# Kernel tuning notes

Measured on AMD Instinct MI355X. Metric: run time of the kernel, lower is better.

The kernel has to match this reference:

```python
import jax, jax.numpy as jnp
import numpy as np

B, CI, HW, K, C, NH, L = 512, 3, 28, 28 // 28 and 0 or 7, 1024, 16, 12
K = 7


def setup_inputs() -> dict:
    key = jax.random.key(0)
    ks = jax.random.split(key, 8)
    s = 0.02
    return {
        "x": jax.random.normal(ks[0], (B, CI, HW, HW), jnp.float32),
        "conv_w": jax.random.normal(ks[1], (C, CI, K, K), jnp.float32) * s,  # Conv2d weight [Co,Ci,k,k], shared with deconv
        "ln1_w": jnp.ones((L, C), jnp.float32),
        "ln1_b": jnp.zeros((L, C), jnp.float32),
        "wq": jax.random.normal(ks[2], (L, C, C), jnp.float32) * s,
        "wk": jax.random.normal(ks[3], (L, C, C), jnp.float32) * s,
        "wv": jax.random.normal(ks[4], (L, C, C), jnp.float32) * s,
        "ln2_w": jnp.ones((L, C), jnp.float32),
        "ln2_b": jnp.zeros((L, C), jnp.float32),
        "mlp_w": jax.random.normal(ks[5], (L, C, C), jnp.float32) * s,
        "mlp_b": jnp.zeros((L, C), jnp.float32),
        "out_w": jax.random.normal(ks[6], (C, C), jnp.float32) * s,
        "out_b": jnp.zeros((C,), jnp.float32),
        "head_num": NH,
    }


def _layernorm(x, w, b, eps=1e-5):
    m = jnp.mean(x, axis=-1, keepdims=True)
    v = jnp.var(x, axis=-1, keepdims=True)  # biased var, matches torch LayerNorm
    return (x - m) * jax.lax.rsqrt(v + eps) * w + b


def _attn(h, wq, wk, wv, nh):
    b, t, c = h.shape
    hd = c // nh
    q = (h @ wq.T).reshape(b, t, nh, hd).transpose(0, 2, 1, 3)  # [B,H,T,hd]
    k = (h @ wk.T).reshape(b, t, nh, hd).transpose(0, 2, 1, 3)
    v = (h @ wv.T).reshape(b, t, nh, hd).transpose(0, 2, 1, 3)
    scores = jnp.einsum("bhqd,bhkd->bhqk", q, k) / jnp.sqrt(jnp.float32(hd))
    mask = jnp.tril(jnp.ones((t, t), bool))
    scores = jnp.where(mask, scores, -jnp.inf)
    a = jax.nn.softmax(scores, axis=-1)
    o = jnp.einsum("bhqk,bhkd->bhqd", a, v)
    return o.transpose(0, 2, 1, 3).reshape(b, t, c)


def _forward(x, conv_w, ln1_w, ln1_b, wq, wk, wv, ln2_w, ln2_b, mlp_w, mlp_b, out_w, out_b, head_num):
    b, ci, hh, ww = x.shape
    co, _, k, _ = conv_w.shape
    # thumbnail: bilinear downsample to (k,k) (align_corners=False == half-pixel), then k-strided conv -> [B,Co]
    thumb = jax.image.resize(x, (b, ci, k, k), method="bilinear", antialias=False)
    thumb_tok = jnp.einsum("bcpq,dcpq->bd", thumb, conv_w)
    # kernel==stride conv == patchify + matmul
    hp, wp = hh // k, ww // k
    xp = x.reshape(b, ci, hp, k, wp, k)
    patches = jnp.einsum("bcipjq,dcpq->bdij", xp, conv_w).reshape(b, co, hp * wp)
    h = jnp.concatenate([thumb_tok[:, :, None], patches], axis=-1).transpose(0, 2, 1)  # [B,T=1+hp*wp,C]
    nlayers = ln1_w.shape[0]
    for l in range(nlayers):
        a = _attn(_layernorm(h, ln1_w[l], ln1_b[l]), wq[l], wk[l], wv[l], head_num)
        h = h + a
        m = _layernorm(h, ln2_w[l], ln2_b[l]) @ mlp_w[l].T + mlp_b[l]
        h = h + m
    logits = h @ out_w.T + out_b  # [B,T,C]
    # decode: ConvTranspose2d(kernel=stride=k) with shared weight; input [B,Co,1,T] -> [B,Ci,k,T*k]
    z = logits.transpose(0, 2, 1)  # [B,Co,T]
    t = z.shape[-1]
    out = jnp.einsum("bcs,cdhw->bdhsw", z, conv_w).reshape(b, ci, k, t * k)
    return out


def reference(x, conv_w, ln1_w, ln1_b, wq, wk, wv, ln2_w, ln2_b, mlp_w, mlp_b, out_w, out_b, head_num):
    return _forward(x, conv_w, ln1_w, ln1_b, wq, wk, wv, ln2_w, ln2_b, mlp_w, mlp_b, out_w, out_b, head_num)
```

## Files before the change

### kernel.cpp

```cpp
#include <hip/hip_runtime.h>


typedef unsigned short u16;
typedef short bfrag8 __attribute__((ext_vector_type(8)));
typedef float facc4 __attribute__((ext_vector_type(4)));

__device__ __forceinline__ u16 f2bf(float f) {
  union { float f; unsigned u; } x; x.f = f;
  unsigned r = x.u + 0x7fffu + ((x.u >> 16) & 1u);
  return (u16)(r >> 16);
}
__device__ __forceinline__ float bf2f(u16 h) {
  union { unsigned u; float f; } x; x.u = ((unsigned)h) << 16;
  return x.f;
}

template <int MODE>
__global__ __launch_bounds__(256) void gemm_bt(
    const u16* __restrict__ A, int lda,
    const u16* __restrict__ B0, const u16* __restrict__ B1, const u16* __restrict__ B2,
    int ldb, int K,
    void* __restrict__ outp, long long zstride, int ldo,
    const float* __restrict__ bias)
{
  __shared__ __align__(16) u16 smem[8192];
  u16* const As = smem;
  u16* const Bs = smem + 4096;

  const int m0 = blockIdx.x * 128;
  const int n0 = blockIdx.y * 128;
  const int z  = blockIdx.z;
  const u16* __restrict__ B = (z == 0) ? B0 : ((z == 1) ? B1 : B2);

  const int tid  = threadIdx.x;
  const int wave = tid >> 6;
  const int lane = tid & 63;
  const int wm   = (wave >> 1) * 64;
  const int wn   = (wave & 1) * 64;
  const int lrow = lane & 15;
  const int lquad = lane >> 4;

  facc4 acc[4][4] = {};

  int rA0, g0; { const int rp = tid >> 3, q = tid & 7, qp = q ^ (rp & 3);
                 rA0 = rp * 2 + (qp >> 2); g0 = qp & 3; }
  int rA1, g1; { const int s1 = tid + 256, rp = s1 >> 3, q = s1 & 7, qp = q ^ (rp & 3);
                 rA1 = rp * 2 + (qp >> 2); g1 = qp & 3; }
  const u16* ga0 = A + (long long)(m0 + rA0) * lda + g0 * 8;
  const u16* ga1 = A + (long long)(m0 + rA1) * lda + g1 * 8;
  const u16* gb0 = B + (long long)(n0 + rA0) * ldb + g0 * 8;
  const u16* gb1 = B + (long long)(n0 + rA1) * ldb + g1 * 8;

  const int ra = wm + lrow;
  const int pa = (((ra & 1) << 2) | lquad) ^ ((ra >> 1) & 3);
  const u16* const abase = As + (((ra >> 1) * 8 + pa) << 3);
  const int rb = wn + lrow;
  const int pb = (((rb & 1) << 2) | lquad) ^ ((rb >> 1) & 3);
  const u16* const bbase = Bs + (((rb >> 1) * 8 + pb) << 3);

  for (int k0 = 0; k0 < K; k0 += 32) {
    __builtin_amdgcn_global_load_lds((const __attribute__((address_space(1))) void*)ga0,
                                     (__attribute__((address_space(3))) void*)(As + tid * 8), 16, 0, 0);
    __builtin_amdgcn_global_load_lds((const __attribute__((address_space(1))) void*)ga1,
                                     (__attribute__((address_space(3))) void*)(As + (tid + 256) * 8), 16, 0, 0);
    __builtin_amdgcn_global_load_lds((const __attribute__((address_space(1))) void*)gb0,
                                     (__attribute__((address_space(3))) void*)(Bs + tid * 8), 16, 0, 0);
    __builtin_amdgcn_global_load_lds((const __attribute__((address_space(1))) void*)gb1,
                                     (__attribute__((address_space(3))) void*)(Bs + (tid + 256) * 8), 16, 0, 0);
    ga0 += 32; ga1 += 32; gb0 += 32; gb1 += 32;
    __syncthreads();

    bfrag8 af[4], bfr[4];
#pragma unroll
    for (int im = 0; im < 4; ++im) af[im] = *(const bfrag8*)(abase + 512 * im);
#pragma unroll
    for (int in = 0; in < 4; ++in) bfr[in] = *(const bfrag8*)(bbase + 512 * in);
#pragma unroll
    for (int im = 0; im < 4; ++im)
#pragma unroll
      for (int in = 0; in < 4; ++in)
        acc[im][in] = __builtin_amdgcn_mfma_f32_16x16x32_bf16(af[im], bfr[in], acc[im][in], 0, 0, 0);
    __syncthreads();
  }

  if (MODE == 1) {
    u16* const outb = ((u16*)outp) + zstride * z;
    u16* const Ts = smem;
#pragma unroll
    for (int half = 0; half < 2; ++half) {
      if ((wave >> 1) == half) {
#pragma unroll
        for (int in = 0; in < 4; ++in) {
          const int col = wn + in * 16 + lrow;
          const float bb = bias ? bias[n0 + col] : 0.0f;
#pragma unroll
          for (int im = 0; im < 4; ++im)
#pragma unroll
            for (int r = 0; r < 4; ++r)
              Ts[(im * 16 + lquad * 4 + r) * 128 + col] = f2bf(acc[im][in][r] + bb);
        }
      }
      __syncthreads();
#pragma unroll
      for (int it = 0; it < 4; ++it) {
        const int g = it * 256 + tid;
        const int row = g >> 4, colg = g & 15;
        *(uint4*)(outb + (long long)(m0 + half * 64 + row) * ldo + n0 + colg * 8) =
            *(const uint4*)(Ts + row * 128 + colg * 8);
      }
      __syncthreads();
    }
    return;
  }

#pragma unroll
  for (int in = 0; in < 4; ++in) {
    const int col = n0 + wn + in * 16 + lrow;
    const float bb = (MODE != 3 && bias) ? bias[col] : 0.0f;
#pragma unroll
    for (int im = 0; im < 4; ++im) {
#pragma unroll
      for (int r = 0; r < 4; ++r) {
        const int row = m0 + wm + im * 16 + lquad * 4 + r;
        const float v = acc[im][in][r] + bb;
        if (MODE == 0) {
          ((float*)outp)[(long long)row * ldo + col] = v;
        } else if (MODE == 2) {
          ((float*)outp)[(long long)row * ldo + col] += v;
        } else {
          if (col < 147) {
            const int b = row / 17, s = row - b * 17;
            const int d = col / 49, rem = col - d * 49;
            const int hk = rem / 7, wk = rem - hk * 7;
            ((float*)outp)[(long long)((b * 3 + d) * 7 + hk) * 119 + s * 7 + wk] = v;
          }
        }
      }
    }
  }
}

__global__ __launch_bounds__(256) void ln_kernel(
    const float* __restrict__ h, const float* __restrict__ w,
    const float* __restrict__ b, u16* __restrict__ out)
{
  const long long row = blockIdx.x;
  const float* __restrict__ x = h + row * 1024;
  const int t = threadIdx.x;
  float v0 = x[t], v1 = x[t + 256], v2 = x[t + 512], v3 = x[t + 768];
  float s = v0 + v1 + v2 + v3;
  float q = v0 * v0 + v1 * v1 + v2 * v2 + v3 * v3;
  for (int o = 32; o > 0; o >>= 1) { s += __shfl_down(s, o); q += __shfl_down(q, o); }
  __shared__ float ss[4], sq[4];
  const int wave = t >> 6, lane = t & 63;
  if (lane == 0) { ss[wave] = s; sq[wave] = q; }
  __syncthreads();
  const float st = ss[0] + ss[1] + ss[2] + ss[3];
  const float qt = sq[0] + sq[1] + sq[2] + sq[3];
  const float mean = st * (1.0f / 1024.0f);
  const float var = qt * (1.0f / 1024.0f) - mean * mean;
  const float inv = rsqrtf(var + 1e-5f);
  u16* o2 = out + row * 1024;
  o2[t]       = f2bf((v0 - mean) * inv * w[t]       + b[t]);
  o2[t + 256] = f2bf((v1 - mean) * inv * w[t + 256] + b[t + 256]);
  o2[t + 512] = f2bf((v2 - mean) * inv * w[t + 512] + b[t + 512]);
  o2[t + 768] = f2bf((v3 - mean) * inv * w[t + 768] + b[t + 768]);
}

__global__ __launch_bounds__(256) void attn_kernel(const u16* __restrict__ QKV,
                                                   float* __restrict__ h)
{
  const int blk = blockIdx.x;
  const int b = blk >> 4, head = blk & 15;
  __shared__ float qs[17][64], ks[17][64], vs[17][64];
  __shared__ float sc[17][20];
  const long long base = (long long)b * 17 * 1024 + head * 64;
  const u16* Q  = QKV;
  const u16* Kp = QKV + 8912896LL;
  const u16* V  = QKV + 17825792LL;

  for (int i = threadIdx.x; i < 17 * 64; i += 256) {
    const int t = i >> 6, d = i & 63;
    const long long off = base + (long long)t * 1024 + d;
    qs[t][d] = bf2f(Q[off]); ks[t][d] = bf2f(Kp[off]); vs[t][d] = bf2f(V[off]);
  }
  __syncthreads();

  for (int i = threadIdx.x; i < 289; i += 256) {
    const int tq = i / 17, tk = i % 17;
    float a = 0.0f;
    if (tk <= tq) {
#pragma unroll
      for (int d = 0; d < 64; ++d) a += qs[tq][d] * ks[tk][d];
      a *= 0.125f;
    }
    sc[tq][tk] = a;
  }
  __syncthreads();

  if (threadIdx.x < 17) {
    const int tq = threadIdx.x;
    float m = -1e30f;
    for (int tk = 0; tk <= tq; ++tk) m = fmaxf(m, sc[tq][tk]);
    float s = 0.0f;
    for (int tk = 0; tk <= tq; ++tk) { const float e = __expf(sc[tq][tk] - m); sc[tq][tk] = e; s += e; }
    const float inv = 1.0f / s;
    for (int tk = 0; tk <= tq; ++tk) sc[tq][tk] *= inv;
  }
  __syncthreads();

  for (int i = threadIdx.x; i < 17 * 64; i += 256) {
    const int tq = i >> 6, d = i & 63;
    float a = 0.0f;
    for (int tk = 0; tk <= tq; ++tk) a += sc[tq][tk] * vs[tk][d];
    h[base + (long long)tq * 1024 + d] += a;
  }
}

__global__ void build_p(const float* __restrict__ x, u16* __restrict__ P)
{
  const int n = blockIdx.x;
  const int j = threadIdx.x;
  if (j >= 160) return;
  const int b = n / 17, t = n % 17;
  float val = 0.0f;
  if (j < 147) {
    const int c = j / 49, rem = j % 49, p = rem / 7, q = rem % 7;
    const float* xb = x + (long long)(b * 3 + c) * 784;
    if (t == 0) {
      const int r = 4 * p + 1, cc = 4 * q + 1;
      val = 0.25f * (xb[r * 28 + cc] + xb[r * 28 + cc + 1] +
                     xb[(r + 1) * 28 + cc] + xb[(r + 1) * 28 + cc + 1]);
    } else {
      const int s = t - 1, ii = s >> 2, jj = s & 3;
      val = xb[(7 * ii + p) * 28 + 7 * jj + q];
    }
  }
  P[(long long)n * 160 + j] = f2bf(val);
}

__global__ __launch_bounds__(256) void cvt_conv(const float* __restrict__ cw,
                                                u16* __restrict__ Wc, u16* __restrict__ cw2)
{
  const int i = blockIdx.x * 256 + threadIdx.x;
  if (i < 163840) {
    const int d = i / 160, j = i % 160;
    Wc[i] = (j < 147) ? f2bf(cw[d * 147 + j]) : (u16)0;
  } else {
    const int i2 = i - 163840;
    if (i2 < 262144) {
      const int j = i2 / 1024, c = i2 % 1024;
      cw2[i2] = (j < 147) ? f2bf(cw[c * 147 + j]) : (u16)0;
    }
  }
}

__global__ __launch_bounds__(256) void cvt_all(
    const float* __restrict__ wq, const float* __restrict__ wk,
    const float* __restrict__ wv, const float* __restrict__ mlpw,
    const float* __restrict__ outw, u16* __restrict__ wAll)
{
  const int i = blockIdx.x * 256 + threadIdx.x;
  const int which = i >> 18;
  const int off = i & 262143;
  const float4* src;
  if (which < 48) {
    const int layer = which >> 2, sub = which & 3;
    const float* base = (sub == 0) ? wq : (sub == 1) ? wk : (sub == 2) ? wv : mlpw;
    src = (const float4*)(base + (size_t)layer * 1048576) + off;
  } else {
    src = (const float4*)outw + off;
  }
  const float4 v = *src;
  ushort4 o; o.x = f2bf(v.x); o.y = f2bf(v.y); o.z = f2bf(v.z); o.w = f2bf(v.w);
  *(ushort4*)(wAll + (size_t)which * 1048576 + (size_t)off * 4) = o;
}

__global__ __launch_bounds__(256) void cvt4(const float* __restrict__ a0, const float* __restrict__ a1,
                                            const float* __restrict__ a2, const float* __restrict__ a3,
                                            u16* __restrict__ o3, u16* __restrict__ om)
{
  const int i = blockIdx.x * 256 + threadIdx.x;
  const int which = i >> 20, off = i & 1048575;
  const float* src = (which == 0) ? a0 : (which == 1) ? a1 : (which == 2) ? a2 : a3;
  const float v = src[off];
  if (which < 3) o3[which * 1048576 + off] = f2bf(v);
  else           om[off] = f2bf(v);
}

__global__ __launch_bounds__(256) void cvtN(const float* __restrict__ in, u16* __restrict__ out, int n)
{
  const int i = blockIdx.x * 256 + threadIdx.x;
  if (i < n) out[i] = f2bf(in[i]);
}

extern "C" void kernel_launch(void* const* d_in, const int* in_sizes, int n_in,
                              void* d_out, int out_size, void* d_ws, size_t ws_size,
                              hipStream_t stream)
{
  const float* x     = (const float*)d_in[0];
  const float* convw = (const float*)d_in[1];
  const float* ln1w  = (const float*)d_in[2];
  const float* ln1b  = (const float*)d_in[3];
  const float* wq    = (const float*)d_in[4];
  const float* wk    = (const float*)d_in[5];
  const float* wv    = (const float*)d_in[6];
  const float* ln2w  = (const float*)d_in[7];
  const float* ln2b  = (const float*)d_in[8];
  const float* mlpw  = (const float*)d_in[9];
  const float* mlpb  = (const float*)d_in[10];
  const float* outw  = (const float*)d_in[11];
  const float* outb  = (const float*)d_in[12];

  char* w = (char*)d_ws;
  const bool big = (ws_size >= 213352448ULL);

  if (big) {
    float* h   = (float*)(w);
    u16* Abuf  = (u16*)(w + 35651584);
    u16* QKV   = (u16*)(w + 53477376);
    u16* wAll  = (u16*)(w + 106954752);
    u16* Wc    = (u16*)(w + 209715200);
    u16* cw2   = (u16*)(w + 210042880);
    u16* P     = (u16*)(w + 210567168);

    cvt_all<<<50176, 256, 0, stream>>>(wq, wk, wv, mlpw, outw, wAll);
    cvt_conv<<<1664, 256, 0, stream>>>(convw, Wc, cw2);
    build_p<<<8704, 192, 0, stream>>>(x, P);
    gemm_bt<0><<<dim3(68, 8, 1), 256, 0, stream>>>(P, 160, Wc, Wc, Wc, 160, 160,
                                                   (void*)h, 0LL, 1024, nullptr);
    for (int l = 0; l < 12; ++l) {
      u16* wl = wAll + (size_t)l * 4194304;
      ln_kernel<<<8704, 256, 0, stream>>>(h, ln1w + l * 1024, ln1b + l * 1024, Abuf);
      gemm_bt<1><<<dim3(68, 8, 3), 256, 0, stream>>>(Abuf, 1024, wl, wl + 1048576, wl + 2097152,
                                                     1024, 1024, (void*)QKV, 8912896LL, 1024, nullptr);
      attn_kernel<<<8192, 256, 0, stream>>>(QKV, h);
      ln_kernel<<<8704, 256, 0, stream>>>(h, ln2w + l * 1024, ln2b + l * 1024, Abuf);
      gemm_bt<2><<<dim3(68, 8, 1), 256, 0, stream>>>(Abuf, 1024, wl + 3145728, wl, wl,
                                                     1024, 1024, (void*)h, 0LL, 1024, mlpb + l * 1024);
    }
    u16* wout = wAll + (size_t)48 * 1048576;
    cvtN<<<34816, 256, 0, stream>>>(h, Abuf, 8912896);
    gemm_bt<1><<<dim3(68, 8, 1), 256, 0, stream>>>(Abuf, 1024, wout, wout, wout,
                                                   1024, 1024, (void*)QKV, 0LL, 1024, outb);
    gemm_bt<3><<<dim3(68, 2, 1), 256, 0, stream>>>(QKV, 1024, cw2, cw2, cw2,
                                                   1024, 1024, d_out, 0LL, 0, nullptr);
  } else {
    if (ws_size < 118980608ULL) return;
    float* h   = (float*)(w);
    u16* Abuf  = (u16*)(w + 35651584);
    u16* QKV   = (u16*)(w + 53477376);
    u16* wb3   = (u16*)(w + 106954752);
    u16* wmb   = (u16*)(w + 113246208);
    u16* Wc    = (u16*)(w + 115343360);
    u16* cw2   = (u16*)(w + 115671040);
    u16* P     = (u16*)(w + 116195328);

    cvt_conv<<<1664, 256, 0, stream>>>(convw, Wc, cw2);
    build_p<<<8704, 192, 0, stream>>>(x, P);
    gemm_bt<0><<<dim3(68, 8, 1), 256, 0, stream>>>(P, 160, Wc, Wc, Wc, 160, 160,
                                                   (void*)h, 0LL, 1024, nullptr);
    for (int l = 0; l < 12; ++l) {
      const size_t wo = (size_t)l * 1048576;
      cvt4<<<16384, 256, 0, stream>>>(wq + wo, wk + wo, wv + wo, mlpw + wo, wb3, wmb);
      ln_kernel<<<8704, 256, 0, stream>>>(h, ln1w + l * 1024, ln1b + l * 1024, Abuf);
      gemm_bt<1><<<dim3(68, 8, 3), 256, 0, stream>>>(Abuf, 1024, wb3, wb3 + 1048576, wb3 + 2097152,
                                                     1024, 1024, (void*)QKV, 8912896LL, 1024, nullptr);
      attn_kernel<<<8192, 256, 0, stream>>>(QKV, h);
      ln_kernel<<<8704, 256, 0, stream>>>(h, ln2w + l * 1024, ln2b + l * 1024, Abuf);
      gemm_bt<2><<<dim3(68, 8, 1), 256, 0, stream>>>(Abuf, 1024, wmb, wmb, wmb,
                                                     1024, 1024, (void*)h, 0LL, 1024, mlpb + l * 1024);
    }
    cvtN<<<34816, 256, 0, stream>>>(h, Abuf, 8912896);
    cvtN<<<4096, 256, 0, stream>>>(outw, wmb, 1048576);
    gemm_bt<1><<<dim3(68, 8, 1), 256, 0, stream>>>(Abuf, 1024, wmb, wmb, wmb,
                                                   1024, 1024, (void*)QKV, 0LL, 1024, outb);
    gemm_bt<3><<<dim3(68, 2, 1), 256, 0, stream>>>(QKV, 1024, cw2, cw2, cw2,
                                                   1024, 1024, d_out, 0LL, 0, nullptr);
  }
}
```

Before: 3.052 ms.

## Use K=64 GEMM tiles, swap grid order, drop LDS swizzle and staged bf16 store

The bf16 GEMM now loads a 64-wide K slice per iteration into separate A/B shared buffers, which halves the number of barrier pairs per tile. The grid is reordered so blockIdx.x walks N, letting consecutive blocks share the same A rows. The XOR-swizzled LDS layout is replaced with a plain row layout, and the LDS-staged coalesced bf16 epilogue for MODE 1 is replaced with direct scalar stores. The patch-embedding K is padded to 192 to fit the new tile depth. The plain layout risks LDS bank conflicts, and the scalar bf16 stores are uncoalesced.

```diff
diff --git a/kernel.cpp b/kernel.cpp
--- a/kernel.cpp
+++ b/kernel.cpp
@@ -23,12 +23,11 @@
     void* __restrict__ outp, long long zstride, int ldo,
     const float* __restrict__ bias)
 {
-  __shared__ __align__(16) u16 smem[8192];
-  u16* const As = smem;
-  u16* const Bs = smem + 4096;
-
-  const int m0 = blockIdx.x * 128;
-  const int n0 = blockIdx.y * 128;
+  __shared__ __align__(16) u16 As[8192];
+  __shared__ __align__(16) u16 Bs[8192];
+
+  const int n0 = blockIdx.x * 128;
+  const int m0 = blockIdx.y * 128;
   const int z  = blockIdx.z;
   const u16* __restrict__ B = (z == 0) ? B0 : ((z == 1) ? B1 : B2);
 
@@ -42,75 +41,44 @@
 
   facc4 acc[4][4] = {};
 
-  int rA0, g0; { const int rp = tid >> 3, q = tid & 7, qp = q ^ (rp & 3);
-                 rA0 = rp * 2 + (qp >> 2); g0 = qp & 3; }
-  int rA1, g1; { const int s1 = tid + 256, rp = s1 >> 3, q = s1 & 7, qp = q ^ (rp & 3);
-                 rA1 = rp * 2 + (qp >> 2); g1 = qp & 3; }
-  const u16* ga0 = A + (long long)(m0 + rA0) * lda + g0 * 8;
-  const u16* ga1 = A + (long long)(m0 + rA1) * lda + g1 * 8;
-  const u16* gb0 = B + (long long)(n0 + rA0) * ldb + g0 * 8;
-  const u16* gb1 = B + (long long)(n0 + rA1) * ldb + g1 * 8;
-
-  const int ra = wm + lrow;
-  const int pa = (((ra & 1) << 2) | lquad) ^ ((ra >> 1) & 3);
-  const u16* const abase = As + (((ra >> 1) * 8 + pa) << 3);
-  const int rb = wn + lrow;
-  const int pb = (((rb & 1) << 2) | lquad) ^ ((rb >> 1) & 3);
-  const u16* const bbase = Bs + (((rb >> 1) * 8 + pb) << 3);
-
-  for (int k0 = 0; k0 < K; k0 += 32) {
-    __builtin_amdgcn_global_load_lds((const __attribute__((address_space(1))) void*)ga0,
-                                     (__attribute__((address_space(3))) void*)(As + tid * 8), 16, 0, 0);
-    __builtin_amdgcn_global_load_lds((const __attribute__((address_space(1))) void*)ga1,
-                                     (__attribute__((address_space(3))) void*)(As + (tid + 256) * 8), 16, 0, 0);
-    __builtin_amdgcn_global_load_lds((const __attribute__((address_space(1))) void*)gb0,
-                                     (__attribute__((address_space(3))) void*)(Bs + tid * 8), 16, 0, 0);
-    __builtin_amdgcn_global_load_lds((const __attribute__((address_space(1))) void*)gb1,
-                                     (__attribute__((address_space(3))) void*)(Bs + (tid + 256) * 8), 16, 0, 0);
-    ga0 += 32; ga1 += 32; gb0 += 32; gb1 += 32;
+  const u16* ga[4]; const u16* gb[4];
+#pragma unroll
+  for (int j = 0; j < 4; ++j) {
+    const int s = tid + 256 * j;
+    const int t = s >> 9, s2 = s & 511;
+    const int r = s2 >> 2, c = (s2 & 3) + 4 * t;
+    ga[j] = A + (long long)(m0 + r) * lda + c * 8;
+    gb[j] = B + (long long)(n0 + r) * ldb + c * 8;
+  }
+
+  const int aoff = (wm + lrow) * 32 + lquad * 8;
+  const int boff = (wn + lrow) * 32 + lquad * 8;
+
+  for (int k0 = 0; k0 < K; k0 += 64) {
+#pragma unroll
+    for (int j = 0; j < 4; ++j) {
+      __builtin_amdgcn_global_load_lds((const __attribute__((address_space(1))) void*)ga[j],
+                                       (__attribute__((address_space(3))) void*)(As + (tid + 256 * j) * 8), 16, 0, 0);
+      __builtin_amdgcn_global_load_lds((const __attribute__((address_space(1))) void*)gb[j],
+                                       (__attribute__((address_space(3))) void*)(Bs + (tid + 256 * j) * 8), 16, 0, 0);
+      ga[j] += 64; gb[j] += 64;
+    }
     __syncthreads();
 
-    bfrag8 af[4], bfr[4];
-#pragma unroll
-    for (int im = 0; im < 4; ++im) af[im] = *(const bfrag8*)(abase + 512 * im);
-#pragma unroll
-    for (int in = 0; in < 4; ++in) bfr[in] = *(const bfrag8*)(bbase + 512 * in);
-#pragma unroll
-    for (int im = 0; im < 4; ++im)
-#pragma unroll
-      for (int in = 0; in < 4; ++in)
-        acc[im][in] = __builtin_amdgcn_mfma_f32_16x16x32_bf16(af[im], bfr[in], acc[im][in], 0, 0, 0);
+#pragma unroll
+    for (int t = 0; t < 2; ++t) {
+      bfrag8 af[4], bfr[4];
+#pragma unroll
+      for (int im = 0; im < 4; ++im) af[im] = *(const bfrag8*)(As + t * 4096 + aoff + 512 * im);
+#pragma unroll
+      for (int in = 0; in < 4; ++in) bfr[in] = *(const bfrag8*)(Bs + t * 4096 + boff + 512 * in);
+#pragma unroll
+      for (int im = 0; im < 4; ++im)
+#pragma unroll
+        for (int in = 0; in < 4; ++in)
+          acc[im][in] = __builtin_amdgcn_mfma_f32_16x16x32_bf16(af[im], bfr[in], acc[im][in], 0, 0, 0);
+    }
     __syncthreads();
-  }
-
-  if (MODE == 1) {
-    u16* const outb = ((u16*)outp) + zstride * z;
-    u16* const Ts = smem;
-#pragma unroll
-    for (int half = 0; half < 2; ++half) {
-      if ((wave >> 1) == half) {
-#pragma unroll
-        for (int in = 0; in < 4; ++in) {
-          const int col = wn + in * 16 + lrow;
-          const float bb = bias ? bias[n0 + col] : 0.0f;
-#pragma unroll
-          for (int im = 0; im < 4; ++im)
-#pragma unroll
-            for (int r = 0; r < 4; ++r)
-              Ts[(im * 16 + lquad * 4 + r) * 128 + col] = f2bf(acc[im][in][r] + bb);
-        }
-      }
-      __syncthreads();
-#pragma unroll
-      for (int it = 0; it < 4; ++it) {
-        const int g = it * 256 + tid;
-        const int row = g >> 4, colg = g & 15;
-        *(uint4*)(outb + (long long)(m0 + half * 64 + row) * ldo + n0 + colg * 8) =
-            *(const uint4*)(Ts + row * 128 + colg * 8);
-      }
-      __syncthreads();
-    }
-    return;
   }
 
 #pragma unroll
@@ -125,6 +93,8 @@
         const float v = acc[im][in][r] + bb;
         if (MODE == 0) {
           ((float*)outp)[(long long)row * ldo + col] = v;
+        } else if (MODE == 1) {
+          (((u16*)outp) + zstride * z)[(long long)row * ldo + col] = f2bf(v);
         } else if (MODE == 2) {
           ((float*)outp)[(long long)row * ldo + col] += v;
         } else {
@@ -221,7 +191,7 @@
 {
   const int n = blockIdx.x;
   const int j = threadIdx.x;
-  if (j >= 160) return;
+  if (j >= 192) return;
   const int b = n / 17, t = n % 17;
   float val = 0.0f;
   if (j < 147) {
@@ -236,18 +206,18 @@
       val = xb[(7 * ii + p) * 28 + 7 * jj + q];
     }
   }
-  P[(long long)n * 160 + j] = f2bf(val);
+  P[(long long)n * 192 + j] = f2bf(val);
 }
 
 __global__ __launch_bounds__(256) void cvt_conv(const float* __restrict__ cw,
                                                 u16* __restrict__ Wc, u16* __restrict__ cw2)
 {
   const int i = blockIdx.x * 256 + threadIdx.x;
-  if (i < 163840) {
-    const int d = i / 160, j = i % 160;
+  if (i < 196608) {
+    const int d = i / 192, j = i % 192;
     Wc[i] = (j < 147) ? f2bf(cw[d * 147 + j]) : (u16)0;
   } else {
-    const int i2 = i - 163840;
+    const int i2 = i - 196608;
     if (i2 < 262144) {
       const int j = i2 / 1024, c = i2 % 1024;
       cw2[i2] = (j < 147) ? f2bf(cw[c * 147 + j]) : (u16)0;
@@ -313,7 +283,7 @@
   const float* outb  = (const float*)d_in[12];
 
   char* w = (char*)d_ws;
-  const bool big = (ws_size >= 213352448ULL);
+  const bool big = (ws_size >= 213975040ULL);
 
   if (big) {
     float* h   = (float*)(w);
@@ -321,61 +291,61 @@
     u16* QKV   = (u16*)(w + 53477376);
     u16* wAll  = (u16*)(w + 106954752);
     u16* Wc    = (u16*)(w + 209715200);
-    u16* cw2   = (u16*)(w + 210042880);
-    u16* P     = (u16*)(w + 210567168);
+    u16* cw2   = (u16*)(w + 210108416);
+    u16* P     = (u16*)(w + 210632704);
 
     cvt_all<<<50176, 256, 0, stream>>>(wq, wk, wv, mlpw, outw, wAll);
-    cvt_conv<<<1664, 256, 0, stream>>>(convw, Wc, cw2);
+    cvt_conv<<<1792, 256, 0, stream>>>(convw, Wc, cw2);
     build_p<<<8704, 192, 0, stream>>>(x, P);
-    gemm_bt<0><<<dim3(68, 8, 1), 256, 0, stream>>>(P, 160, Wc, Wc, Wc, 160, 160,
+    gemm_bt<0><<<dim3(8, 68, 1), 256, 0, stream>>>(P, 192, Wc, Wc, Wc, 192, 192,
                                                    (void*)h, 0LL, 1024, nullptr);
     for (int l = 0; l < 12; ++l) {
       u16* wl = wAll + (size_t)l * 4194304;
       ln_kernel<<<8704, 256, 0, stream>>>(h, ln1w + l * 1024, ln1b + l * 1024, Abuf);
-      gemm_bt<1><<<dim3(68, 8, 3), 256, 0, stream>>>(Abuf, 1024, wl, wl + 1048576, wl + 2097152,
+      gemm_bt<1><<<dim3(8, 68, 3), 256, 0, stream>>>(Abuf, 1024, wl, wl + 1048576, wl + 2097152,
                                                      1024, 1024, (void*)QKV, 8912896LL, 1024, nullptr);
       attn_kernel<<<8192, 256, 0, stream>>>(QKV, h);
       ln_kernel<<<8704, 256, 0, stream>>>(h, ln2w + l * 1024, ln2b + l * 1024, Abuf);
-      gemm_bt<2><<<dim3(68, 8, 1), 256, 0, stream>>>(Abuf, 1024, wl + 3145728, wl, wl,
+      gemm_bt<2><<<dim3(8, 68, 1), 256, 0, stream>>>(Abuf, 1024, wl + 3145728, wl, wl,
                                                      1024, 1024, (void*)h, 0LL, 1024, mlpb + l * 1024);
     }
     u16* wout = wAll + (size_t)48 * 1048576;
     cvtN<<<34816, 256, 0, stream>>>(h, Abuf, 8912896);
-    gemm_bt<1><<<dim3(68, 8, 1), 256, 0, stream>>>(Abuf, 1024, wout, wout, wout,
+    gemm_bt<1><<<dim3(8, 68, 1), 256, 0, stream>>>(Abuf, 1024, wout, wout, wout,
                                                    1024, 1024, (void*)QKV, 0LL, 1024, outb);
-    gemm_bt<3><<<dim3(68, 2, 1), 256, 0, stream>>>(QKV, 1024, cw2, cw2, cw2,
+    gemm_bt<3><<<dim3(2, 68, 1), 256, 0, stream>>>(QKV, 1024, cw2, cw2, cw2,
                                                    1024, 1024, d_out, 0LL, 0, nullptr);
   } else {
-    if (ws_size < 118980608ULL) return;
+    if (ws_size < 119603200ULL) return;
     float* h   = (float*)(w);
     u16* Abuf  = (u16*)(w + 35651584);
     u16* QKV   = (u16*)(w + 53477376);
     u16* wb3   = (u16*)(w + 106954752);
     u16* wmb   = (u16*)(w + 113246208);
     u16* Wc    = (u16*)(w + 115343360);
-    u16* cw2   = (u16*)(w + 115671040);
-    u16* P     = (u16*)(w + 116195328);
-
-    cvt_conv<<<1664, 256, 0, stream>>>(convw, Wc, cw2);
+    u16* cw2   = (u16*)(w + 115736576);
+    u16* P     = (u16*)(w + 116260864);
+
+    cvt_conv<<<1792, 256, 0, stream>>>(convw, Wc, cw2);
     build_p<<<8704, 192, 0, stream>>>(x, P);
-    gemm_bt<0><<<dim3(68, 8, 1), 256, 0, stream>>>(P, 160, Wc, Wc, Wc, 160, 160,
+    gemm_bt<0><<<dim3(8, 68, 1), 256, 0, stream>>>(P, 192, Wc, Wc, Wc, 192, 192,
                                                    (void*)h, 0LL, 1024, nullptr);
     for (int l = 0; l < 12; ++l) {
       const size_t wo = (size_t)l * 1048576;
       cvt4<<<16384, 256, 0, stream>>>(wq + wo, wk + wo, wv + wo, mlpw + wo, wb3, wmb);
       ln_kernel<<<8704, 256, 0, stream>>>(h, ln1w + l * 1024, ln1b + l * 1024, Abuf);
-      gemm_bt<1><<<dim3(68, 8, 3), 256, 0, stream>>>(Abuf, 1024, wb3, wb3 + 1048576, wb3 + 2097152,
+      gemm_bt<1><<<dim3(8, 68, 3), 256, 0, stream>>>(Abuf, 1024, wb3, wb3 + 1048576, wb3 + 2097152,
                                                      1024, 1024, (void*)QKV, 8912896LL, 1024, nullptr);
       attn_kernel<<<8192, 256, 0, stream>>>(QKV, h);
       ln_kernel<<<8704, 256, 0, stream>>>(h, ln2w + l * 1024, ln2b + l * 1024, Abuf);
-      gemm_bt<2><<<dim3(68, 8, 1), 256, 0, stream>>>(Abuf, 1024, wmb, wmb, wmb,
+      gemm_bt<2><<<dim3(8, 68, 1), 256, 0, stream>>>(Abuf, 1024, wmb, wmb, wmb,
                                                      1024, 1024, (void*)h, 0LL, 1024, mlpb + l * 1024);
     }
     cvtN<<<34816, 256, 0, stream>>>(h, Abuf, 8912896);
     cvtN<<<4096, 256, 0, stream>>>(outw, wmb, 1048576);
-    gemm_bt<1><<<dim3(68, 8, 1), 256, 0, stream>>>(Abuf, 1024, wmb, wmb, wmb,
+    gemm_bt<1><<<dim3(8, 68, 1), 256, 0, stream>>>(Abuf, 1024, wmb, wmb, wmb,
                                                    1024, 1024, (void*)QKV, 0LL, 1024, outb);
-    gemm_bt<3><<<dim3(68, 2, 1), 256, 0, stream>>>(QKV, 1024, cw2, cw2, cw2,
+    gemm_bt<3><<<dim3(2, 68, 1), 256, 0, stream>>>(QKV, 1024, cw2, cw2, cw2,
                                                    1024, 1024, d_out, 0LL, 0, nullptr);
   }
 }
```

Result: faster. 2.970 ms (-2.7%).
